# Optimization experiments

Measured on AMD Instinct MI355X. Metric: run time of the kernel, lower is better.

Reference implementation:

```python
import jax, jax.numpy as jnp
import numpy as np

B = 8192          # batch_size (pairs of embeddings)
D = 1024          # embedding dim
C = 1024          # number of classes (torch.unique(labels) -> 0..C-1, all present)
EPS = 1e-12       # F.normalize eps


def _normalize(x):
    # F.normalize(x, dim=1): x / max(||x||_2, eps)
    n = jnp.linalg.norm(x, axis=1, keepdims=True)
    return x / jnp.maximum(n, EPS)


def setup_inputs() -> dict:
    key = jax.random.key(0)
    k1, k2, k3 = jax.random.split(key, 3)
    emb_i = jax.random.normal(k1, (B, D), dtype=jnp.float32)
    emb_j = jax.random.normal(k2, (B, D), dtype=jnp.float32)
    # shuffled arange % C guarantees every class id in [0, C) appears,
    # matching torch.unique(labels) == arange(C)
    labels = jax.random.permutation(k3, jnp.arange(B, dtype=jnp.int32) % C).astype(jnp.int64)
    return {"emb_i": emb_i, "emb_j": emb_j, "labels": labels}


def reference(emb_i, emb_j, labels):
    z_i = _normalize(emb_i)  # [B, D]
    z_j = _normalize(emb_j)  # [B, D]

    # vectorized replacement of the per-label python loop:
    # class_prototypes[c] = mean of z_i rows with label c  (segment mean)
    seg_sum = jax.ops.segment_sum(z_i, labels, num_segments=C)                    # [C, D]
    seg_cnt = jax.ops.segment_sum(jnp.ones((B,), z_i.dtype), labels, num_segments=C)  # [C]
    prototypes = seg_sum / seg_cnt[:, None]                                       # [C, D]

    # similarity = 2 - cdist(z_j, prototypes, p=2)
    d2 = (jnp.sum(z_j * z_j, axis=1)[:, None]
          + jnp.sum(prototypes * prototypes, axis=1)[None, :]
          - 2.0 * z_j @ prototypes.T)                                             # [B, C]
    sim = 2.0 - jnp.sqrt(jnp.maximum(d2, 0.0))

    # match_matrix: labels_proto (arange(C)) == labels[:, None]
    match = (jnp.arange(C)[None, :] == labels[:, None]).astype(sim.dtype)         # [B, C]

    # BCEWithLogitsLoss (mean reduction), numerically stable via log_sigmoid
    loss = jnp.mean(-(match * jax.nn.log_sigmoid(sim)
                      + (1.0 - match) * jax.nn.log_sigmoid(-sim)))
    return loss
```

## Files before the change

kernel.cpp:

```cpp
#include <hip/hip_runtime.h>

#define B_N 8192
#define D_N 1024
#define C_N 1024
#define BM 128
#define BN 128
#define BK 64

typedef __attribute__((ext_vector_type(8))) __bf16 bf16x8;
typedef __attribute__((ext_vector_type(4))) float floatx4;

__device__ inline unsigned short f2bf(float f) {
  union { float f; unsigned int u; } cv; cv.f = f;
  unsigned int b = cv.u;
  unsigned int r = (b + 0x7FFFu + ((b >> 16) & 1u)) >> 16;
  return (unsigned short)r;
}
__device__ inline float d4(const float4 a) {
  return a.x * a.x + a.y * a.y + a.z * a.z + a.w * a.w;
}
__device__ inline ushort4 pk4(const float4 v, const float s) {
  ushort4 u;
  u.x = f2bf(v.x * s); u.y = f2bf(v.y * s);
  u.z = f2bf(v.z * s); u.w = f2bf(v.w * s);
  return u;
}

__global__ __launch_bounds__(256) void prep_kernel(
    const float* __restrict__ emb_i, const float* __restrict__ emb_j,
    const int* __restrict__ labels,
    unsigned short* __restrict__ z_j, unsigned short* __restrict__ proto,
    float* __restrict__ p2, float* __restrict__ out) {
  __shared__ float sx[4][8];
  __shared__ int list[8];
  __shared__ int scnt;

  const int t = threadIdx.x;
  const int lane = t & 63;
  const int wid = t >> 6;
  const int blk = blockIdx.x;

  if (t == 0) scnt = 0;
  if (blk == 0 && t == 0) out[0] = 0.0f;

#pragma unroll
  for (int it = 0; it < 2; ++it) {
    const int row = blk * 8 + it * 4 + wid;
    const float4* src = (const float4*)(emb_j + (size_t)row * D_N);
    const float4 v0 = src[lane], v1 = src[lane + 64];
    const float4 v2 = src[lane + 128], v3 = src[lane + 192];
    float ss = d4(v0) + d4(v1) + d4(v2) + d4(v3);
    for (int o = 32; o; o >>= 1) ss += __shfl_xor(ss, o, 64);
    const float inv = 1.0f / fmaxf(sqrtf(ss), 1e-12f);
    ushort4* dst = (ushort4*)(z_j + (size_t)row * D_N);
    dst[lane] = pk4(v0, inv);
    dst[lane + 64] = pk4(v1, inv);
    dst[lane + 128] = pk4(v2, inv);
    dst[lane + 192] = pk4(v3, inv);
  }

  const int c = blk;
  __syncthreads();
  const int4* lab4 = (const int4*)labels;
  for (int i = 0; i < 8; ++i) {
    const int q = i * 256 + t;
    const int4 L = lab4[q];
    const int base = q * 4;
    if (L.x == c) list[atomicAdd(&scnt, 1) & 7] = base;
    if (L.y == c) list[atomicAdd(&scnt, 1) & 7] = base + 1;
    if (L.z == c) list[atomicAdd(&scnt, 1) & 7] = base + 2;
    if (L.w == c) list[atomicAdd(&scnt, 1) & 7] = base + 3;
  }
  __syncthreads();

  const float* base = emb_i + wid * 256;
  float4 v[8];
  float ss[8];
#pragma unroll
  for (int k = 0; k < 8; ++k) {
    v[k] = ((const float4*)(base + (size_t)list[k] * D_N))[lane];
    ss[k] = d4(v[k]);
  }
#pragma unroll
  for (int k = 0; k < 8; ++k)
    for (int o = 32; o; o >>= 1) ss[k] += __shfl_xor(ss[k], o, 64);
  if (lane == 0) {
#pragma unroll
    for (int k = 0; k < 8; ++k) sx[wid][k] = ss[k];
  }
  __syncthreads();

  float4 a = make_float4(0.f, 0.f, 0.f, 0.f);
#pragma unroll
  for (int k = 0; k < 8; ++k) {
    const float tot = sx[0][k] + sx[1][k] + sx[2][k] + sx[3][k];
    const float iv = 1.0f / fmaxf(sqrtf(tot), 1e-12f);
    a.x += v[k].x * iv; a.y += v[k].y * iv;
    a.z += v[k].z * iv; a.w += v[k].w * iv;
  }
  a.x *= 0.125f; a.y *= 0.125f; a.z *= 0.125f; a.w *= 0.125f;

  float pp = d4(a);
  for (int o = 32; o; o >>= 1) pp += __shfl_xor(pp, o, 64);
  __syncthreads();
  if (lane == 0) sx[wid][0] = pp;
  __syncthreads();
  if (t == 0) p2[c] = sx[0][0] + sx[1][0] + sx[2][0] + sx[3][0];

  ((ushort4*)(proto + (size_t)c * D_N + wid * 256))[lane] = pk4(a, 1.0f);
}

__global__ __launch_bounds__(256) void gemm_loss_kernel(
    const unsigned short* __restrict__ Zj,
    const unsigned short* __restrict__ P,
    const float* __restrict__ p2,
    const int* __restrict__ labels,
    float* __restrict__ out) {
  __shared__ __align__(16) unsigned short As[BM * BK];
  __shared__ __align__(16) unsigned short Bs[BN * BK];
  __shared__ float sred[4];

  const int t = threadIdx.x;
  const int lane = t & 63;
  const int wid = t >> 6;
  const int wm = (wid >> 1) * 64;
  const int wn = (wid & 1) * 64;
  const int bm = blockIdx.x;
  const int bn = blockIdx.y;

  floatx4 acc[4][4];
#pragma unroll
  for (int i = 0; i < 4; ++i)
#pragma unroll
    for (int j = 0; j < 4; ++j)
      acc[i][j] = (floatx4){0.f, 0.f, 0.f, 0.f};

  const int srow = t >> 3;
  const int scol = (((t & 7) ^ (srow & 7)) << 3);
  const unsigned short* Ag = Zj + (size_t)(bm * BM + srow) * D_N + scol;
  const unsigned short* Bg = P + (size_t)(bn * BN + srow) * D_N + scol;
  unsigned short* Al = As + t * 8;
  unsigned short* Bl = Bs + t * 8;

  for (int k0 = 0; k0 < D_N; k0 += BK) {
#pragma unroll
    for (int it = 0; it < 4; ++it) {
      __builtin_amdgcn_global_load_lds(
          (const __attribute__((address_space(1))) void*)(Ag + (size_t)it * 32 * D_N + k0),
          (__attribute__((address_space(3))) void*)(Al + it * 2048), 16, 0, 0);
      __builtin_amdgcn_global_load_lds(
          (const __attribute__((address_space(1))) void*)(Bg + (size_t)it * 32 * D_N + k0),
          (__attribute__((address_space(3))) void*)(Bl + it * 2048), 16, 0, 0);
    }
    __syncthreads();
#pragma unroll
    for (int kk = 0; kk < BK; kk += 32) {
      const int swz = ((((kk >> 3) + (lane >> 4)) ^ (lane & 7)) << 3);
      bf16x8 af[4], bfr[4];
#pragma unroll
      for (int mi = 0; mi < 4; ++mi)
        af[mi] = *(const bf16x8*)(As + (wm + mi * 16 + (lane & 15)) * BK + swz);
#pragma unroll
      for (int ni = 0; ni < 4; ++ni)
        bfr[ni] = *(const bf16x8*)(Bs + (wn + ni * 16 + (lane & 15)) * BK + swz);
#pragma unroll
      for (int mi = 0; mi < 4; ++mi)
#pragma unroll
        for (int ni = 0; ni < 4; ++ni)
          acc[mi][ni] = __builtin_amdgcn_mfma_f32_16x16x32_bf16(af[mi], bfr[ni], acc[mi][ni], 0, 0, 0);
    }
    __syncthreads();
  }

  const int colb = bn * BN + wn + (lane & 15);
  const int rowb = bm * BM + wm + ((lane >> 4) << 2);
  float p2c[4];
#pragma unroll
  for (int ni = 0; ni < 4; ++ni) p2c[ni] = p2[colb + ni * 16];

  float lsum = 0.f;
#pragma unroll
  for (int mi = 0; mi < 4; ++mi) {
#pragma unroll
    for (int r = 0; r < 4; ++r) {
      const int row = rowb + mi * 16 + r;
      const int lab = labels[row];
#pragma unroll
      for (int ni = 0; ni < 4; ++ni) {
        const float dot = acc[mi][ni][r];
        const float d2 = 1.0f + p2c[ni] - 2.0f * dot;
        const float s = 2.0f - sqrtf(fmaxf(d2, 0.0f));
        const float sp = fmaxf(s, 0.0f) + log1pf(expf(-fabsf(s)));
        lsum += sp - ((lab == colb + ni * 16) ? s : 0.0f);
      }
    }
  }
  for (int o = 32; o; o >>= 1) lsum += __shfl_xor(lsum, o, 64);
  if (lane == 0) sred[wid] = lsum;
  __syncthreads();
  if (t == 0)
    atomicAdd(out, (sred[0] + sred[1] + sred[2] + sred[3]) *
                       (1.0f / ((float)B_N * (float)C_N)));
}

extern "C" void kernel_launch(void* const* d_in, const int* in_sizes, int n_in,
                              void* d_out, int out_size, void* d_ws, size_t ws_size,
                              hipStream_t stream) {
  const float* emb_i = (const float*)d_in[0];
  const float* emb_j = (const float*)d_in[1];
  const int* labels = (const int*)d_in[2];
  float* out = (float*)d_out;

  char* ws = (char*)d_ws;
  unsigned short* z_j = (unsigned short*)ws;
  unsigned short* proto = (unsigned short*)(ws + (size_t)16777216);
  float* p2 = (float*)(ws + (size_t)18874368);

  prep_kernel<<<dim3(C_N), 256, 0, stream>>>(emb_i, emb_j, labels, z_j,
                                             proto, p2, out);
  gemm_loss_kernel<<<dim3(B_N / BM, C_N / BN), 256, 0, stream>>>(z_j, proto,
                                                                 p2, labels, out);
}
```

Measured before the change: 147.4 us.

## Switch GEMM to 32x32x16 MFMA with BK=128 tiles

```diff
diff --git a/kernel.cpp b/kernel.cpp
--- a/kernel.cpp
+++ b/kernel.cpp
@@ -5,10 +5,10 @@
 #define C_N 1024
 #define BM 128
 #define BN 128
-#define BK 64
+#define BK 128
 
 typedef __attribute__((ext_vector_type(8))) __bf16 bf16x8;
-typedef __attribute__((ext_vector_type(4))) float floatx4;
+typedef __attribute__((ext_vector_type(16))) float floatx16;
 
 __device__ inline unsigned short f2bf(float f) {
   union { float f; unsigned int u; } cv; cv.f = f;
@@ -128,70 +128,73 @@
   const int bm = blockIdx.x;
   const int bn = blockIdx.y;
 
-  floatx4 acc[4][4];
-#pragma unroll
-  for (int i = 0; i < 4; ++i)
-#pragma unroll
-    for (int j = 0; j < 4; ++j)
-      acc[i][j] = (floatx4){0.f, 0.f, 0.f, 0.f};
-
-  const int srow = t >> 3;
-  const int scol = (((t & 7) ^ (srow & 7)) << 3);
-  const unsigned short* Ag = Zj + (size_t)(bm * BM + srow) * D_N + scol;
-  const unsigned short* Bg = P + (size_t)(bn * BN + srow) * D_N + scol;
+  floatx16 acc[2][2];
+#pragma unroll
+  for (int i = 0; i < 2; ++i)
+#pragma unroll
+    for (int j = 0; j < 2; ++j)
+      for (int r = 0; r < 16; ++r) acc[i][j][r] = 0.f;
+
+  const int srow = t >> 4;
+  const int g = (t & 15) ^ (srow & 7);
+  const unsigned short* Ag = Zj + (size_t)(bm * BM + srow) * D_N + g * 8;
+  const unsigned short* Bg = P + (size_t)(bn * BN + srow) * D_N + g * 8;
   unsigned short* Al = As + t * 8;
   unsigned short* Bl = Bs + t * 8;
 
+  const int ar0 = (wm + (lane & 31)) * BK;
+  const int ar1 = (wm + 32 + (lane & 31)) * BK;
+  const int br0 = (wn + (lane & 31)) * BK;
+  const int br1 = (wn + 32 + (lane & 31)) * BK;
+  const int h = lane >> 5;
+  const int q = lane & 7;
+
   for (int k0 = 0; k0 < D_N; k0 += BK) {
 #pragma unroll
-    for (int it = 0; it < 4; ++it) {
+    for (int it = 0; it < 8; ++it) {
       __builtin_amdgcn_global_load_lds(
-          (const __attribute__((address_space(1))) void*)(Ag + (size_t)it * 32 * D_N + k0),
+          (const __attribute__((address_space(1))) void*)(Ag + (size_t)it * 16 * D_N + k0),
           (__attribute__((address_space(3))) void*)(Al + it * 2048), 16, 0, 0);
       __builtin_amdgcn_global_load_lds(
-          (const __attribute__((address_space(1))) void*)(Bg + (size_t)it * 32 * D_N + k0),
+          (const __attribute__((address_space(1))) void*)(Bg + (size_t)it * 16 * D_N + k0),
           (__attribute__((address_space(3))) void*)(Bl + it * 2048), 16, 0, 0);
     }
     __syncthreads();
 #pragma unroll
-    for (int kk = 0; kk < BK; kk += 32) {
-      const int swz = ((((kk >> 3) + (lane >> 4)) ^ (lane & 7)) << 3);
-      bf16x8 af[4], bfr[4];
-#pragma unroll
-      for (int mi = 0; mi < 4; ++mi)
-        af[mi] = *(const bf16x8*)(As + (wm + mi * 16 + (lane & 15)) * BK + swz);
-#pragma unroll
-      for (int ni = 0; ni < 4; ++ni)
-        bfr[ni] = *(const bf16x8*)(Bs + (wn + ni * 16 + (lane & 15)) * BK + swz);
-#pragma unroll
-      for (int mi = 0; mi < 4; ++mi)
-#pragma unroll
-        for (int ni = 0; ni < 4; ++ni)
-          acc[mi][ni] = __builtin_amdgcn_mfma_f32_16x16x32_bf16(af[mi], bfr[ni], acc[mi][ni], 0, 0, 0);
+    for (int kk8 = 0; kk8 < 8; ++kk8) {
+      const int swz = (((kk8 * 2 + h) ^ q)) << 3;
+      bf16x8 a0 = *(const bf16x8*)(As + ar0 + swz);
+      bf16x8 a1 = *(const bf16x8*)(As + ar1 + swz);
+      bf16x8 b0 = *(const bf16x8*)(Bs + br0 + swz);
+      bf16x8 b1 = *(const bf16x8*)(Bs + br1 + swz);
+      acc[0][0] = __builtin_amdgcn_mfma_f32_32x32x16_bf16(a0, b0, acc[0][0], 0, 0, 0);
+      acc[0][1] = __builtin_amdgcn_mfma_f32_32x32x16_bf16(a0, b1, acc[0][1], 0, 0, 0);
+      acc[1][0] = __builtin_amdgcn_mfma_f32_32x32x16_bf16(a1, b0, acc[1][0], 0, 0, 0);
+      acc[1][1] = __builtin_amdgcn_mfma_f32_32x32x16_bf16(a1, b1, acc[1][1], 0, 0, 0);
     }
     __syncthreads();
   }
 
-  const int colb = bn * BN + wn + (lane & 15);
-  const int rowb = bm * BM + wm + ((lane >> 4) << 2);
-  float p2c[4];
-#pragma unroll
-  for (int ni = 0; ni < 4; ++ni) p2c[ni] = p2[colb + ni * 16];
-
+  const int colbase = bn * BN + wn + (lane & 31);
   float lsum = 0.f;
 #pragma unroll
-  for (int mi = 0; mi < 4; ++mi) {
-#pragma unroll
-    for (int r = 0; r < 4; ++r) {
-      const int row = rowb + mi * 16 + r;
-      const int lab = labels[row];
-#pragma unroll
-      for (int ni = 0; ni < 4; ++ni) {
-        const float dot = acc[mi][ni][r];
-        const float d2 = 1.0f + p2c[ni] - 2.0f * dot;
+  for (int mb = 0; mb < 2; ++mb) {
+    const int rowbase = bm * BM + wm + mb * 32 + 4 * h;
+    int labv[16];
+#pragma unroll
+    for (int reg = 0; reg < 16; ++reg)
+      labv[reg] = labels[rowbase + (reg & 3) + 8 * (reg >> 2)];
+#pragma unroll
+    for (int nb = 0; nb < 2; ++nb) {
+      const int col = colbase + nb * 32;
+      const float p2c = p2[col];
+#pragma unroll
+      for (int reg = 0; reg < 16; ++reg) {
+        const float dot = acc[mb][nb][reg];
+        const float d2 = 1.0f + p2c - 2.0f * dot;
         const float s = 2.0f - sqrtf(fmaxf(d2, 0.0f));
         const float sp = fmaxf(s, 0.0f) + log1pf(expf(-fabsf(s)));
-        lsum += sp - ((lab == colb + ni * 16) ? s : 0.0f);
+        lsum += sp - ((labv[reg] == col) ? s : 0.0f);
       }
     }
   }
```

New measurement: 146.0 us. Within noise of the previous version (-1.0%).

## Fuse emb_j bf16 conversion into GEMM and apply row norms in epilogue

Applied to the files above, without the earlier changes.

```diff
diff --git a/kernel.cpp b/kernel.cpp
--- a/kernel.cpp
+++ b/kernel.cpp
@@ -8,6 +8,7 @@
 #define BK 64
 
 typedef __attribute__((ext_vector_type(8))) __bf16 bf16x8;
+typedef __attribute__((ext_vector_type(4))) __bf16 bf16x4;
 typedef __attribute__((ext_vector_type(4))) float floatx4;
 
 __device__ inline unsigned short f2bf(float f) {
@@ -29,7 +30,7 @@
 __global__ __launch_bounds__(256) void prep_kernel(
     const float* __restrict__ emb_i, const float* __restrict__ emb_j,
     const int* __restrict__ labels,
-    unsigned short* __restrict__ z_j, unsigned short* __restrict__ proto,
+    float* __restrict__ rn, unsigned short* __restrict__ proto,
     float* __restrict__ p2, float* __restrict__ out) {
   __shared__ float sx[4][8];
   __shared__ int list[8];
@@ -47,16 +48,10 @@
   for (int it = 0; it < 2; ++it) {
     const int row = blk * 8 + it * 4 + wid;
     const float4* src = (const float4*)(emb_j + (size_t)row * D_N);
-    const float4 v0 = src[lane], v1 = src[lane + 64];
-    const float4 v2 = src[lane + 128], v3 = src[lane + 192];
-    float ss = d4(v0) + d4(v1) + d4(v2) + d4(v3);
+    float ss = d4(src[lane]) + d4(src[lane + 64]) +
+               d4(src[lane + 128]) + d4(src[lane + 192]);
     for (int o = 32; o; o >>= 1) ss += __shfl_xor(ss, o, 64);
-    const float inv = 1.0f / fmaxf(sqrtf(ss), 1e-12f);
-    ushort4* dst = (ushort4*)(z_j + (size_t)row * D_N);
-    dst[lane] = pk4(v0, inv);
-    dst[lane + 64] = pk4(v1, inv);
-    dst[lane + 128] = pk4(v2, inv);
-    dst[lane + 192] = pk4(v3, inv);
+    if (lane == 0) rn[row] = 1.0f / fmaxf(sqrtf(ss), 1e-12f);
   }
 
   const int c = blk;
@@ -111,13 +106,15 @@
 }
 
 __global__ __launch_bounds__(256) void gemm_loss_kernel(
-    const unsigned short* __restrict__ Zj,
+    const float* __restrict__ Ej,
     const unsigned short* __restrict__ P,
+    const float* __restrict__ rn,
     const float* __restrict__ p2,
     const int* __restrict__ labels,
     float* __restrict__ out) {
   __shared__ __align__(16) unsigned short As[BM * BK];
   __shared__ __align__(16) unsigned short Bs[BN * BK];
+  __shared__ float srn[BM];
   __shared__ float sred[4];
 
   const int t = threadIdx.x;
@@ -128,6 +125,8 @@
   const int bm = blockIdx.x;
   const int bn = blockIdx.y;
 
+  if (t < BM) srn[t] = rn[bm * BM + t];
+
   floatx4 acc[4][4];
 #pragma unroll
   for (int i = 0; i < 4; ++i)
@@ -137,21 +136,29 @@
 
   const int srow = t >> 3;
   const int scol = (((t & 7) ^ (srow & 7)) << 3);
-  const unsigned short* Ag = Zj + (size_t)(bm * BM + srow) * D_N + scol;
   const unsigned short* Bg = P + (size_t)(bn * BN + srow) * D_N + scol;
-  unsigned short* Al = As + t * 8;
   unsigned short* Bl = Bs + t * 8;
 
+  const float4* Agp = (const float4*)(Ej + (size_t)(bm * BM + (t >> 4)) * D_N) + (t & 15);
+  unsigned short* Aw = As + (t >> 4) * 64 +
+                       ((((t & 15) >> 1) ^ ((t >> 4) & 7)) << 3) + (t & 1) * 4;
+
   for (int k0 = 0; k0 < D_N; k0 += BK) {
 #pragma unroll
     for (int it = 0; it < 4; ++it) {
-      __builtin_amdgcn_global_load_lds(
-          (const __attribute__((address_space(1))) void*)(Ag + (size_t)it * 32 * D_N + k0),
-          (__attribute__((address_space(3))) void*)(Al + it * 2048), 16, 0, 0);
       __builtin_amdgcn_global_load_lds(
           (const __attribute__((address_space(1))) void*)(Bg + (size_t)it * 32 * D_N + k0),
           (__attribute__((address_space(3))) void*)(Bl + it * 2048), 16, 0, 0);
     }
+    const int kq = k0 >> 2;
+#pragma unroll
+    for (int k = 0; k < 8; ++k) {
+      const float4 w = Agp[k * 4096 + kq];
+      bf16x4 bv;
+      bv[0] = (__bf16)w.x; bv[1] = (__bf16)w.y;
+      bv[2] = (__bf16)w.z; bv[3] = (__bf16)w.w;
+      *(bf16x4*)(Aw + k * 1024) = bv;
+    }
     __syncthreads();
 #pragma unroll
     for (int kk = 0; kk < BK; kk += 32) {
@@ -173,7 +180,7 @@
   }
 
   const int colb = bn * BN + wn + (lane & 15);
-  const int rowb = bm * BM + wm + ((lane >> 4) << 2);
+  const int rowloc = wm + ((lane >> 4) << 2);
   float p2c[4];
 #pragma unroll
   for (int ni = 0; ni < 4; ++ni) p2c[ni] = p2[colb + ni * 16];
@@ -183,11 +190,12 @@
   for (int mi = 0; mi < 4; ++mi) {
 #pragma unroll
     for (int r = 0; r < 4; ++r) {
-      const int row = rowb + mi * 16 + r;
-      const int lab = labels[row];
+      const int rl = rowloc + mi * 16 + r;
+      const float rv = srn[rl];
+      const int lab = labels[bm * BM + rl];
 #pragma unroll
       for (int ni = 0; ni < 4; ++ni) {
-        const float dot = acc[mi][ni][r];
+        const float dot = acc[mi][ni][r] * rv;
         const float d2 = 1.0f + p2c[ni] - 2.0f * dot;
         const float s = 2.0f - sqrtf(fmaxf(d2, 0.0f));
         const float sp = fmaxf(s, 0.0f) + log1pf(expf(-fabsf(s)));
@@ -212,12 +220,12 @@
   float* out = (float*)d_out;
 
   char* ws = (char*)d_ws;
-  unsigned short* z_j = (unsigned short*)ws;
-  unsigned short* proto = (unsigned short*)(ws + (size_t)16777216);
-  float* p2 = (float*)(ws + (size_t)18874368);
-
-  prep_kernel<<<dim3(C_N), 256, 0, stream>>>(emb_i, emb_j, labels, z_j,
+  float* rn = (float*)ws;
+  unsigned short* proto = (unsigned short*)(ws + (size_t)32768);
+  float* p2 = (float*)(ws + (size_t)32768 + 2097152);
+
+  prep_kernel<<<dim3(C_N), 256, 0, stream>>>(emb_i, emb_j, labels, rn,
                                              proto, p2, out);
-  gemm_loss_kernel<<<dim3(B_N / BM, C_N / BN), 256, 0, stream>>>(z_j, proto,
-                                                                 p2, labels, out);
-}
+  gemm_loss_kernel<<<dim3(B_N / BM, C_N / BN), 256, 0, stream>>>(emb_j, proto,
+                                                                 rn, p2, labels, out);
+}
```

New measurement: 151.9 us. 3.1% more time.
